# Performance work log

Hardware: AMD Instinct MI355X
Metric: run time of the kernel (lower is better)

## Reference

```python
import jax, jax.numpy as jnp
import numpy as np

TOP_K = 2
NUM_EXPERTS = 8


def setup_inputs() -> dict:
    key = jax.random.key(0)
    ks = jax.random.split(key, 8)
    B, S, H, F, E = 2, 2048, 1024, 4096, NUM_EXPERTS
    x = jax.random.normal(ks[0], (B, S, H), dtype=jnp.float32)
    # Router linear (TopKRouter): hidden -> num_experts
    Wr = jax.random.normal(ks[1], (H, E), dtype=jnp.float32) * 0.02
    br = jnp.zeros((E,), dtype=jnp.float32)
    # Per-expert FeedForwardExpert: Linear(H,F) -> relu -> Linear(F,H), stacked over experts
    W1 = jax.random.normal(ks[2], (E, H, F), dtype=jnp.float32) * 0.02
    b1 = jnp.zeros((E, F), dtype=jnp.float32)
    W2 = jax.random.normal(ks[3], (E, F, H), dtype=jnp.float32) * 0.02
    b2 = jnp.zeros((E, H), dtype=jnp.float32)
    return {"x": x, "Wr": Wr, "br": br, "W1": W1, "b1": b1, "W2": W2, "b2": b2}


def reference(x, Wr, br, W1, b1, W2, b2):
    """MoELayer.forward (eval mode, no dropout, capacity assumed sufficient so
    no random token dropping -- dropping in the original is randperm-based).
    Top-2 routing with renormalized top-k softmax probs, weighted combine."""
    B, S, H = x.shape
    E = Wr.shape[1]
    xf = x.reshape(-1, H)                                   # [T, H]
    logits = xf @ Wr + br                                   # [T, E]
    probs = jax.nn.softmax(logits, axis=-1)
    top_vals, top_idx = jax.lax.top_k(probs, TOP_K)         # [T, k]
    weights = top_vals / jnp.sum(top_vals, axis=-1, keepdims=True)
    # combine weight per (token, expert): sum over k slots assigned to e
    onehot = jax.nn.one_hot(top_idx, E, dtype=xf.dtype)     # [T, k, E]
    combine = jnp.einsum('tk,tke->te', weights, onehot)     # [T, E]
    out = jnp.zeros_like(xf)
    for e in range(E):  # small fixed loop over experts
        h = jax.nn.relu(xf @ W1[e] + b1[e]) @ W2[e] + b2[e]  # [T, H]
        out = out + combine[:, e:e + 1] * h
    return out.reshape(B, S, H)
```

## Files before the change

### kernel.cpp

```cpp
#include <hip/hip_runtime.h>

#define T_TOK 4096
#define H_DIM 1024
#define F_DIM 4096
#define E_NUM 8
#define R_TOT 8192
#define NT_MAX 72
#define R_CAP (NT_MAX * 128)

typedef short bf16x8 __attribute__((ext_vector_type(8)));
typedef float f32x4 __attribute__((ext_vector_type(4)));

__device__ inline unsigned short f2bf(float f) {
  unsigned int u = __builtin_bit_cast(unsigned int, f);
  return (unsigned short)((u + 0x7FFFu + ((u >> 16) & 1u)) >> 16);
}

__device__ inline void async16(const void* g, void* l) {
  __builtin_amdgcn_global_load_lds((const __attribute__((address_space(1))) void*)g,
                                   (__attribute__((address_space(3))) void*)l, 16, 0, 0);
}

__global__ __launch_bounds__(256) void prep_k(
    const float* __restrict__ W1, const float* __restrict__ W2,
    unsigned short* __restrict__ WT1, unsigned short* __restrict__ WT2,
    unsigned short* __restrict__ xg, int* __restrict__ ctrl) {
  int bid = blockIdx.x;
  if (bid >= 16384) {
    int z = bid - 16384;
    if (z < 576) {
      uint4* p = (uint4*)((char*)xg + (size_t)z * 32768) + threadIdx.x * 8;
      uint4 zz = make_uint4(0, 0, 0, 0);
#pragma unroll
      for (int j = 0; j < 8; j++) p[j] = zz;
    } else {
      for (int i = threadIdx.x; i < 1024; i += 256) ctrl[i] = 0;
    }
    return;
  }
  size_t mat = (size_t)H_DIM * F_DIM;
  const float* in; unsigned short* out; int R, C, c0, r0;
  if (bid < 8192) {
    int e = bid >> 10, t = bid & 1023;
    in = W1 + e * mat; out = WT1 + e * mat; R = H_DIM; C = F_DIM;
    c0 = (t & 63) * 64; r0 = (t >> 6) * 64;
  } else {
    int e = (bid - 8192) >> 10, t = bid & 1023;
    in = W2 + e * mat; out = WT2 + e * mat; R = F_DIM; C = H_DIM;
    c0 = (t & 15) * 64; r0 = (t >> 4) * 64;
  }
  __shared__ float tile[64][65];
  int tr = threadIdx.x >> 4, tc = (threadIdx.x & 15) * 4;
#pragma unroll
  for (int p = 0; p < 4; p++) {
    int r = tr + p * 16;
    float4 v = *(const float4*)(in + (size_t)(r0 + r) * C + c0 + tc);
    tile[r][tc + 0] = v.x; tile[r][tc + 1] = v.y;
    tile[r][tc + 2] = v.z; tile[r][tc + 3] = v.w;
  }
  __syncthreads();
  int col = threadIdx.x >> 2;
  int rb  = (threadIdx.x & 3) * 8;
  unsigned short* ob = out + (size_t)(c0 + col) * R + r0;
#pragma unroll
  for (int j = 0; j < 2; j++) {
    int r8 = rb + j * 32;
    uint4 o;
    o.x = (unsigned int)f2bf(tile[r8 + 0][col]) | ((unsigned int)f2bf(tile[r8 + 1][col]) << 16);
    o.y = (unsigned int)f2bf(tile[r8 + 2][col]) | ((unsigned int)f2bf(tile[r8 + 3][col]) << 16);
    o.z = (unsigned int)f2bf(tile[r8 + 4][col]) | ((unsigned int)f2bf(tile[r8 + 5][col]) << 16);
    o.w = (unsigned int)f2bf(tile[r8 + 6][col]) | ((unsigned int)f2bf(tile[r8 + 7][col]) << 16);
    *(uint4*)(ob + r8) = o;
  }
}

__global__ __launch_bounds__(256) void router_k(
    const float* __restrict__ x, const float* __restrict__ Wr,
    const float* __restrict__ br, int* __restrict__ ctrl,
    int* __restrict__ t2i, float* __restrict__ t2w) {
  int lane = threadIdx.x & 63;
  int wid  = threadIdx.x >> 6;
  int t = blockIdx.x * 4 + wid;
  const float* xr = x + (size_t)t * H_DIM;
  double acc[E_NUM];
#pragma unroll
  for (int e = 0; e < E_NUM; e++) acc[e] = 0.0;
  for (int i = lane; i < H_DIM; i += 64) {
    float xv = xr[i];
    const float* wr = Wr + (size_t)i * E_NUM;
    float4 w0 = *(const float4*)wr;
    float4 w1 = *(const float4*)(wr + 4);
    acc[0] += (double)xv * w0.x; acc[1] += (double)xv * w0.y;
    acc[2] += (double)xv * w0.z; acc[3] += (double)xv * w0.w;
    acc[4] += (double)xv * w1.x; acc[5] += (double)xv * w1.y;
    acc[6] += (double)xv * w1.z; acc[7] += (double)xv * w1.w;
  }
#pragma unroll
  for (int e = 0; e < E_NUM; e++) {
    double v = acc[e];
    for (int off = 32; off > 0; off >>= 1) v += __shfl_down(v, off);
    acc[e] = v;
  }
  if (lane == 0) {
    float l[E_NUM];
#pragma unroll
    for (int e = 0; e < E_NUM; e++) l[e] = (float)acc[e] + br[e];
    int ia = 0; float la = l[0];
#pragma unroll
    for (int e = 1; e < E_NUM; e++) if (l[e] > la) { la = l[e]; ia = e; }
    int ib = -1; float lb = -3.4e38f;
#pragma unroll
    for (int e = 0; e < E_NUM; e++) if (e != ia && l[e] > lb) { lb = l[e]; ib = e; }
    float w0 = 1.f / (1.f + __expf(lb - la));
    float w1 = 1.f - w0;
    t2i[2 * t] = ia; t2i[2 * t + 1] = ib;
    t2w[2 * t] = w0; t2w[2 * t + 1] = w1;
    atomicAdd(&ctrl[ia], 1);
    atomicAdd(&ctrl[ib], 1);
  }
}

__global__ void scan_k(int* ctrl) {
  int lane = threadIdx.x;
  int c = (lane < 8) ? ctrl[lane] : 0;
  int tiles = (c + 127) >> 7;
  int x = tiles;
  for (int d = 1; d < 8; d <<= 1) {
    int y = __shfl_up(x, d);
    if (lane >= d) x += y;
  }
  int excl = x - tiles;
  if (lane < 8) {
    ctrl[8 + lane]  = excl * 128;
    ctrl[17 + lane] = excl * 128;
  }
  int tot = __shfl(x, 7);
  if (lane == 0) { ctrl[25] = tot; ctrl[16] = tot * 128; }
  int ex[8], tl[8];
#pragma unroll
  for (int e = 0; e < 8; e++) { ex[e] = __shfl(excl, e); tl[e] = __shfl(tiles, e); }
  for (int i = lane; i < tot; i += 64) {
    int myE = 0;
#pragma unroll
    for (int e = 0; e < 8; e++) if (i >= ex[e] && i < ex[e] + tl[e]) myE = e;
    ctrl[32 + 2 * i] = myE;
    ctrl[33 + 2 * i] = i * 128;
  }
}

__global__ __launch_bounds__(256) void assign_k(
    const int* __restrict__ t2i, int* __restrict__ ctrl, int* __restrict__ row_map) {
  int g = blockIdx.x * 256 + threadIdx.x;
  int lane = threadIdx.x & 63;
  int e = t2i[g];
  int row = 0;
#pragma unroll
  for (int ee = 0; ee < E_NUM; ee++) {
    unsigned long long mask = __ballot(e == ee);
    if (e == ee) {
      int leader = __ffsll((long long)mask) - 1;
      int cnt = __popcll(mask);
      int rank = __popcll(mask & ((lane == 63) ? ~0ull >> 1 << 1 >> 1 | ((1ull << 63) - 1) & ((1ull << lane) - 1) : ((1ull << lane) - 1)));
      int base = 0;
      if (lane == leader) base = atomicAdd(&ctrl[17 + ee], cnt);
      base = __shfl(base, leader);
      row = base + rank;
    }
  }
  row_map[g] = row;
}

__global__ __launch_bounds__(128) void gcopy_k(
    const float* __restrict__ x, const int* __restrict__ row_map,
    unsigned short* __restrict__ xg) {
  int bid = blockIdx.x;
  int row = row_map[bid];
  int t = bid >> 1;
  const float* src = x + (size_t)t * H_DIM + threadIdx.x * 8;
  unsigned short* dst = xg + (size_t)row * H_DIM + threadIdx.x * 8;
  float4 v0 = *(const float4*)src;
  float4 v1 = *(const float4*)(src + 4);
  uint4 o;
  o.x = (unsigned int)f2bf(v0.x) | ((unsigned int)f2bf(v0.y) << 16);
  o.y = (unsigned int)f2bf(v0.z) | ((unsigned int)f2bf(v0.w) << 16);
  o.z = (unsigned int)f2bf(v1.x) | ((unsigned int)f2bf(v1.y) << 16);
  o.w = (unsigned int)f2bf(v1.z) | ((unsigned int)f2bf(v1.w) << 16);
  *(uint4*)dst = o;
}

#define BAR() do { __builtin_amdgcn_sched_barrier(0); \
                   __builtin_amdgcn_s_barrier(); \
                   __builtin_amdgcn_sched_barrier(0); } while (0)

#define STG(gbase, kt, ebase, c) \
  async16((gbase) + (size_t)((c) * 32 + srcRow) * Kstr + (kt) + srcK8, \
          lds + (ebase) + (c) * 2048 + tid * 8)

#define LDU(ebase, row, koct) \
  (*(const bf16x8*)(lds + (ebase) + (((row) * 8 + ((koct) ^ ((row) & 7))) * 8)))

template <int MAP, bool RELU, bool OUTF32>
__global__ __launch_bounds__(256, 2) void gemm128_k(
    const int* __restrict__ ctrl, const unsigned short* __restrict__ A,
    const unsigned short* __restrict__ Bw, const float* __restrict__ bias,
    void* __restrict__ Cout, int Kstr, int N) {
  __shared__ unsigned short lds[32768];
  const int bid = blockIdx.x;
  int rt, bx;
  if (MAP == 1) {
    int wg = (bid & 7) * 288 + (bid >> 3);
    rt = wg >> 5; bx = wg & 31;
  } else {
    int wg = (bid & 7) * 72 + (bid >> 3);
    rt = wg >> 3; bx = wg & 7;
  }
  if (rt >= ctrl[25]) return;
  const int e    = ctrl[32 + 2 * rt];
  const int row0 = ctrl[33 + 2 * rt];
  const unsigned short* Ae = A + (size_t)row0 * Kstr;
  const unsigned short* Be = Bw + (size_t)e * ((size_t)N * Kstr) + (size_t)bx * 128 * Kstr;
  const int tid = threadIdx.x, lane = tid & 63;
  const int wid = tid >> 6, wm = wid >> 1, wn = wid & 1;
  const int lr = lane & 15, klane = lane >> 4;
  const int srcRow = tid >> 3;
  const int srcK8  = ((tid & 7) ^ (srcRow & 7)) * 8;
  const int NT = Kstr >> 6;

  f32x4 acc[4][4];
  f32x4 zero4 = {0.f, 0.f, 0.f, 0.f};
#pragma unroll
  for (int m = 0; m < 4; m++)
#pragma unroll
    for (int n = 0; n < 4; n++) acc[m][n] = zero4;

  {
    STG(Ae, 0, 0, 0); STG(Ae, 0, 0, 1); STG(Ae, 0, 0, 2); STG(Ae, 0, 0, 3);
    STG(Be, 0, 8192, 0); STG(Be, 0, 8192, 1); STG(Be, 0, 8192, 2); STG(Be, 0, 8192, 3);
    STG(Ae, 64, 16384, 0); STG(Ae, 64, 16384, 1); STG(Ae, 64, 16384, 2); STG(Ae, 64, 16384, 3);
    STG(Be, 64, 24576, 0); STG(Be, 64, 24576, 1); STG(Be, 64, 24576, 2); STG(Be, 64, 24576, 3);
    asm volatile("s_waitcnt vmcnt(8)" ::: "memory");
    BAR();
  }

  for (int t = 0; t < NT; t++) {
    const int cur = t & 1;
    const int abase = cur * 16384;
    const int bbase = abase + 8192;
    const int kt2 = min(t + 2, NT - 1) * 64;
    bf16x8 a[4][2], b[4][2];
#pragma unroll
    for (int m = 0; m < 4; m++) {
      int ar = wm * 64 + m * 16 + lr;
      a[m][0] = LDU(abase, ar, klane);
      a[m][1] = LDU(abase, ar, 4 + klane);
    }
#pragma unroll
    for (int n = 0; n < 4; n++) {
      int br = wn * 64 + n * 16 + lr;
      b[n][0] = LDU(bbase, br, klane);
      b[n][1] = LDU(bbase, br, 4 + klane);
    }
    asm volatile("s_waitcnt lgkmcnt(0)" ::: "memory");
    BAR();
    STG(Ae, kt2, abase, 0); STG(Ae, kt2, abase, 1);
    STG(Ae, kt2, abase, 2); STG(Ae, kt2, abase, 3);
    STG(Be, kt2, bbase, 0); STG(Be, kt2, bbase, 1);
    STG(Be, kt2, bbase, 2); STG(Be, kt2, bbase, 3);
    __builtin_amdgcn_s_setprio(1);
#pragma unroll
    for (int m = 0; m < 4; m++)
#pragma unroll
      for (int n = 0; n < 4; n++) {
        acc[m][n] = __builtin_amdgcn_mfma_f32_16x16x32_bf16(a[m][0], b[n][0], acc[m][n], 0, 0, 0);
        acc[m][n] = __builtin_amdgcn_mfma_f32_16x16x32_bf16(a[m][1], b[n][1], acc[m][n], 0, 0, 0);
      }
    __builtin_amdgcn_s_setprio(0);
    asm volatile("s_waitcnt vmcnt(8)" ::: "memory");
    BAR();
  }

  const int n0 = bx * 128;
  const float* be = bias + (size_t)e * N;
#pragma unroll
  for (int m = 0; m < 4; m++) {
#pragma unroll
    for (int q2 = 0; q2 < 4; q2++) {
      size_t ro = (size_t)(row0 + wm * 64 + m * 16 + (lane >> 4) * 4 + q2) * N;
#pragma unroll
      for (int n = 0; n < 4; n++) {
        int col = n0 + wn * 64 + n * 16 + lr;
        float v = acc[m][n][q2] + be[col];
        if (RELU) v = fmaxf(v, 0.f);
        if (OUTF32) ((float*)Cout)[ro + col] = v;
        else ((unsigned short*)Cout)[ro + col] = f2bf(v);
      }
    }
  }
}

__global__ __launch_bounds__(256) void combine_k(
    const float* __restrict__ y, const int* __restrict__ row_map,
    const float* __restrict__ t2w, float* __restrict__ out) {
  int t = blockIdx.x;
  int i = threadIdx.x * 4;
  int r0 = row_map[2 * t], r1 = row_map[2 * t + 1];
  float w0 = t2w[2 * t], w1 = t2w[2 * t + 1];
  float4 a = *(const float4*)(y + (size_t)r0 * H_DIM + i);
  float4 b = *(const float4*)(y + (size_t)r1 * H_DIM + i);
  float4 o;
  o.x = w0 * a.x + w1 * b.x;
  o.y = w0 * a.y + w1 * b.y;
  o.z = w0 * a.z + w1 * b.z;
  o.w = w0 * a.w + w1 * b.w;
  *(float4*)(out + (size_t)t * H_DIM + i) = o;
}

extern "C" void kernel_launch(void* const* d_in, const int* in_sizes, int n_in,
                              void* d_out, int out_size, void* d_ws, size_t ws_size,
                              hipStream_t stream) {
  const float* x  = (const float*)d_in[0];
  const float* Wr = (const float*)d_in[1];
  const float* br = (const float*)d_in[2];
  const float* W1 = (const float*)d_in[3];
  const float* b1 = (const float*)d_in[4];
  const float* W2 = (const float*)d_in[5];
  const float* b2 = (const float*)d_in[6];
  float* out = (float*)d_out;

  char* ws = (char*)d_ws;
  int*   ctrl    = (int*)ws;
  int*   t2i     = (int*)(ws + 4096);
  float* t2w     = (float*)(ws + 4096 + 32768);
  int*   row_map = (int*)(ws + 4096 + 65536);
  size_t off = (size_t)1 << 20;
  unsigned short* WT1 = (unsigned short*)(ws + off); off += (size_t)E_NUM * F_DIM * H_DIM * 2;
  unsigned short* WT2 = (unsigned short*)(ws + off); off += (size_t)E_NUM * H_DIM * F_DIM * 2;
  unsigned short* xg  = (unsigned short*)(ws + off); off += (size_t)R_CAP * H_DIM * 2;
  unsigned short* hb  = (unsigned short*)(ws + off); off += (size_t)R_CAP * F_DIM * 2;
  float*          yb  = (float*)(ws + off);          off += (size_t)R_CAP * H_DIM * 4;

  if (ws_size < off) {
    hipMemsetAsync(d_out, 0, (size_t)out_size * 4, stream);
    return;
  }

  prep_k<<<dim3(16961), 256, 0, stream>>>(W1, W2, WT1, WT2, xg, ctrl);
  router_k<<<dim3(T_TOK / 4), 256, 0, stream>>>(x, Wr, br, ctrl, t2i, t2w);
  scan_k<<<dim3(1), 64, 0, stream>>>(ctrl);
  assign_k<<<dim3(R_TOT / 256), 256, 0, stream>>>(t2i, ctrl, row_map);
  gcopy_k<<<dim3(R_TOT), 128, 0, stream>>>(x, row_map, xg);
  gemm128_k<1, true, false><<<dim3(2304), 256, 0, stream>>>(
      ctrl, xg, WT1, b1, hb, H_DIM, F_DIM);
  gemm128_k<2, false, true><<<dim3(576), 256, 0, stream>>>(
      ctrl, hb, WT2, b2, yb, F_DIM, H_DIM);
  combine_k<<<dim3(T_TOK), 256, 0, stream>>>(yb, row_map, t2w, out);
}
```

Measured before the change: 419.6 us.

## Restructure MoE GEMM main loop into eight-phase interleaved load/compute pipeline

Each pair of K-tiles is now processed in eight phases. Each phase reads a 32x32 quadrant of the warp tile from LDS, issues two async global-to-LDS copies for a future tile, and runs eight MFMAs. The idea is to spread global loads across the compute and keep MFMA issue busy, in the style of HipKittens 8-wave ping-pong. The cost is twice as many barriers per K-tile and finer-grained LDS reads. The LDS buffer-reuse ordering is intricate and must be correct to avoid races.

```diff
diff --git a/kernel.cpp b/kernel.cpp
--- a/kernel.cpp
+++ b/kernel.cpp
@@ -199,8 +199,43 @@
 #define LDU(ebase, row, koct) \
   (*(const bf16x8*)(lds + (ebase) + (((row) * 8 + ((koct) ^ ((row) & 7))) * 8)))
 
+#define MF(A, B, C) __builtin_amdgcn_mfma_f32_16x16x32_bf16(A, B, C, 0, 0, 0)
+
+#define PHASE(Q, RB, G, EB, C0, C1, KT, VM) \
+  { \
+    const int qr = (Q) & 1, qc = ((Q) >> 1) & 1; \
+    const int arow = wm * 64 + qr * 32 + lr; \
+    const int brow = wn * 64 + qc * 32 + lr; \
+    bf16x8 aA = LDU((RB), arow, klane); \
+    bf16x8 aB = LDU((RB), arow, 4 + klane); \
+    bf16x8 aC = LDU((RB), arow + 16, klane); \
+    bf16x8 aD = LDU((RB), arow + 16, 4 + klane); \
+    bf16x8 bA = LDU((RB) + 8192, brow, klane); \
+    bf16x8 bB = LDU((RB) + 8192, brow, 4 + klane); \
+    bf16x8 bC = LDU((RB) + 8192, brow + 16, klane); \
+    bf16x8 bD = LDU((RB) + 8192, brow + 16, 4 + klane); \
+    STG((G), (KT), (EB), (C0)); \
+    STG((G), (KT), (EB), (C1)); \
+    BAR(); \
+    asm volatile("s_waitcnt lgkmcnt(0)" ::: "memory"); \
+    __builtin_amdgcn_sched_barrier(0); \
+    __builtin_amdgcn_s_setprio(1); \
+    { const int mi = qr * 2, ni = qc * 2; \
+      acc[mi][ni]         = MF(aA, bA, acc[mi][ni]); \
+      acc[mi][ni]         = MF(aB, bB, acc[mi][ni]); \
+      acc[mi][ni + 1]     = MF(aA, bC, acc[mi][ni + 1]); \
+      acc[mi][ni + 1]     = MF(aB, bD, acc[mi][ni + 1]); \
+      acc[mi + 1][ni]     = MF(aC, bA, acc[mi + 1][ni]); \
+      acc[mi + 1][ni]     = MF(aD, bB, acc[mi + 1][ni]); \
+      acc[mi + 1][ni + 1] = MF(aC, bC, acc[mi + 1][ni + 1]); \
+      acc[mi + 1][ni + 1] = MF(aD, bD, acc[mi + 1][ni + 1]); } \
+    __builtin_amdgcn_s_setprio(0); \
+    if (VM) { asm volatile("s_waitcnt vmcnt(2)" ::: "memory"); } \
+    BAR(); \
+  }
+
 template <int MAP, bool RELU, bool OUTF32>
-__global__ __launch_bounds__(256, 2) void gemm128_k(
+__global__ __launch_bounds__(256, 2) void gemm8p_k(
     const int* __restrict__ ctrl, const unsigned short* __restrict__ A,
     const unsigned short* __restrict__ Bw, const float* __restrict__ bias,
     void* __restrict__ Cout, int Kstr, int N) {
@@ -225,6 +260,7 @@
   const int srcRow = tid >> 3;
   const int srcK8  = ((tid & 7) ^ (srcRow & 7)) * 8;
   const int NT = Kstr >> 6;
+  const int NI = NT >> 1;
 
   f32x4 acc[4][4];
   f32x4 zero4 = {0.f, 0.f, 0.f, 0.f};
@@ -236,47 +272,23 @@
   {
     STG(Ae, 0, 0, 0); STG(Ae, 0, 0, 1); STG(Ae, 0, 0, 2); STG(Ae, 0, 0, 3);
     STG(Be, 0, 8192, 0); STG(Be, 0, 8192, 1); STG(Be, 0, 8192, 2); STG(Be, 0, 8192, 3);
-    STG(Ae, 64, 16384, 0); STG(Ae, 64, 16384, 1); STG(Ae, 64, 16384, 2); STG(Ae, 64, 16384, 3);
-    STG(Be, 64, 24576, 0); STG(Be, 64, 24576, 1); STG(Be, 64, 24576, 2); STG(Be, 64, 24576, 3);
-    asm volatile("s_waitcnt vmcnt(8)" ::: "memory");
+    STG(Ae, 64, 16384, 0); STG(Ae, 64, 16384, 2);
+    asm volatile("s_waitcnt vmcnt(2)" ::: "memory");
     BAR();
   }
 
-  for (int t = 0; t < NT; t++) {
-    const int cur = t & 1;
-    const int abase = cur * 16384;
-    const int bbase = abase + 8192;
-    const int kt2 = min(t + 2, NT - 1) * 64;
-    bf16x8 a[4][2], b[4][2];
-#pragma unroll
-    for (int m = 0; m < 4; m++) {
-      int ar = wm * 64 + m * 16 + lr;
-      a[m][0] = LDU(abase, ar, klane);
-      a[m][1] = LDU(abase, ar, 4 + klane);
-    }
-#pragma unroll
-    for (int n = 0; n < 4; n++) {
-      int br = wn * 64 + n * 16 + lr;
-      b[n][0] = LDU(bbase, br, klane);
-      b[n][1] = LDU(bbase, br, 4 + klane);
-    }
-    asm volatile("s_waitcnt lgkmcnt(0)" ::: "memory");
-    BAR();
-    STG(Ae, kt2, abase, 0); STG(Ae, kt2, abase, 1);
-    STG(Ae, kt2, abase, 2); STG(Ae, kt2, abase, 3);
-    STG(Be, kt2, bbase, 0); STG(Be, kt2, bbase, 1);
-    STG(Be, kt2, bbase, 2); STG(Be, kt2, bbase, 3);
-    __builtin_amdgcn_s_setprio(1);
-#pragma unroll
-    for (int m = 0; m < 4; m++)
-#pragma unroll
-      for (int n = 0; n < 4; n++) {
-        acc[m][n] = __builtin_amdgcn_mfma_f32_16x16x32_bf16(a[m][0], b[n][0], acc[m][n], 0, 0, 0);
-        acc[m][n] = __builtin_amdgcn_mfma_f32_16x16x32_bf16(a[m][1], b[n][1], acc[m][n], 0, 0, 0);
-      }
-    __builtin_amdgcn_s_setprio(0);
-    asm volatile("s_waitcnt vmcnt(8)" ::: "memory");
-    BAR();
+  for (int i = 0; i < NI; i++) {
+    const int kt1 = (2 * i + 1) * 64;
+    const int kt2 = min(2 * i + 2, NT - 1) * 64;
+    const int kt3 = min(2 * i + 3, NT - 1) * 64;
+    PHASE(0, 0,     Ae, 16384, 1, 3, kt1, 0)
+    PHASE(1, 0,     Be, 24576, 0, 1, kt1, 0)
+    PHASE(2, 0,     Be, 24576, 2, 3, kt1, 0)
+    PHASE(3, 0,     Ae, 0,     0, 2, kt2, 1)
+    PHASE(4, 16384, Ae, 0,     1, 3, kt2, 0)
+    PHASE(5, 16384, Be, 8192,  0, 1, kt2, 0)
+    PHASE(6, 16384, Be, 8192,  2, 3, kt2, 0)
+    PHASE(7, 16384, Ae, 16384, 0, 2, kt3, 1)
   }
 
   const int n0 = bx * 128;
@@ -349,9 +361,9 @@
   scan_k<<<dim3(1), 64, 0, stream>>>(ctrl);
   assign_k<<<dim3(R_TOT / 256), 256, 0, stream>>>(t2i, ctrl, row_map);
   gcopy_k<<<dim3(R_TOT), 128, 0, stream>>>(x, row_map, xg);
-  gemm128_k<1, true, false><<<dim3(2304), 256, 0, stream>>>(
+  gemm8p_k<1, true, false><<<dim3(2304), 256, 0, stream>>>(
       ctrl, xg, WT1, b1, hb, H_DIM, F_DIM);
-  gemm128_k<2, false, true><<<dim3(576), 256, 0, stream>>>(
+  gemm8p_k<2, false, true><<<dim3(576), 256, 0, stream>>>(
       ctrl, hb, WT2, b2, yb, F_DIM, H_DIM);
   combine_k<<<dim3(T_TOK), 256, 0, stream>>>(yb, row_map, t2w, out);
 }
```

After: 450.3 us. +7.3%, slower.
